# Kernel optimization log

Hardware: AMD Instinct MI355X
Metric: run time of the kernel (lower is better)

The kernel has to match this reference:

```python
import jax, jax.numpy as jnp
import numpy as np

N = 100000      # nodes
E = 800000      # edges
P = 200000      # number of subgraph permutations
L = 16          # lrp_length
D = 64          # lrp_out_dim (== lrp_in_dim)
PL = P * L
LEN_SEQ = 4     # int(sqrt(L))
NUM_BOND = 4


def setup_inputs() -> dict:
    key = jax.random.key(0)
    ks = jax.random.split(key, 16)
    inp = {}
    inp["nfeat"] = jax.random.normal(ks[0], (N, D), jnp.float32)
    inp["degs"] = jax.random.uniform(ks[1], (N,), jnp.float32) * 8.0 + 1.0
    inp["n2p_val"] = jnp.ones((PL,), jnp.float32)
    inp["e2p_val"] = jnp.ones((PL,), jnp.float32)
    inp["pool_val"] = jax.random.uniform(ks[2], (P,), jnp.float32)
    inp["weights"] = jax.random.normal(ks[3], (D, D, L), jnp.float32)
    inp["bias"] = jnp.zeros((1, D), jnp.float32)
    inp["w_deg0"] = jax.random.normal(ks[4], (2 * D, LEN_SEQ), jnp.float32) * 0.3
    inp["b_deg0"] = jnp.zeros((2 * D,), jnp.float32)
    inp["w_deg1"] = jax.random.normal(ks[5], (D, 2 * D), jnp.float32) * 0.1
    inp["b_deg1"] = jnp.zeros((D,), jnp.float32)
    inp["w_lin"] = jax.random.normal(ks[6], (D, D), jnp.float32) * 0.1
    inp["b_lin"] = jnp.zeros((D,), jnp.float32)
    inp["bond_emb"] = jax.random.normal(ks[7], (NUM_BOND, D), jnp.float32)
    inp["edge_feat_idx"] = jax.random.randint(ks[8], (E,), 0, NUM_BOND, jnp.int32)
    inp["n2p_row"] = jnp.arange(PL, dtype=jnp.int32)
    inp["n2p_col"] = jax.random.randint(ks[9], (PL,), 0, N, jnp.int32)
    inp["e2p_row"] = jnp.arange(PL, dtype=jnp.int32)
    inp["e2p_col"] = jax.random.randint(ks[10], (PL,), 0, E, jnp.int32)
    inp["pool_row"] = jax.random.randint(ks[11], (P,), 0, N, jnp.int32)
    inp["pool_col"] = jnp.arange(P, dtype=jnp.int32)
    return inp


def _spmm(row, col, val, x, m):
    # COO spmm: out[r] = sum_{nnz with row==r} val * x[col]
    return jax.ops.segment_sum(val[:, None] * x[col], row, num_segments=m)


def reference(nfeat, degs, n2p_val, e2p_val, pool_val, weights, bias,
              w_deg0, b_deg0, w_deg1, b_deg1, w_lin, b_lin, bond_emb,
              edge_feat_idx, n2p_row, n2p_col, e2p_row, e2p_col,
              pool_row, pool_col):
    n = nfeat.shape[0]
    pl = n2p_row.shape[0]
    d = weights.shape[0]
    l = weights.shape[2]
    p = pl // l
    len_seq = int(round(l ** 0.5))

    efeat = bond_emb[edge_feat_idx]                                  # [E, D]
    perm = _spmm(n2p_row, n2p_col, n2p_val, nfeat, pl) \
         + _spmm(e2p_row, e2p_col, e2p_val, efeat, pl)               # [P*L, D]
    deg_perm = _spmm(n2p_row, n2p_col, n2p_val, degs[:, None], pl)   # [P*L, 1]

    x = perm.reshape(p, l, d)                                        # [P, L, D]
    deg_sel = deg_perm.reshape(p, l)[:, ::len_seq + 1]               # [P, len_seq]

    h = jnp.einsum('pab,bca->pc', x, weights) + bias                 # [P, D]
    h = jax.nn.relu(h) @ w_lin.T + b_lin                             # linear(relu(.))

    g = jax.nn.relu(deg_sel @ w_deg0.T + b_deg0) @ w_deg1.T + b_deg1  # [P, D]
    h = h * g

    out = _spmm(pool_row, pool_col, pool_val, h, n)                  # [N, D]
    return out
```

## Files before the change

### kernel.cpp

```cpp
#include <hip/hip_runtime.h>
#include <hip/hip_bf16.h>

typedef __attribute__((ext_vector_type(8))) __bf16 bf16x8;
typedef __attribute__((ext_vector_type(4))) float floatx4;
typedef __attribute__((ext_vector_type(4))) int intx4;
typedef __attribute__((ext_vector_type(4))) unsigned uintx4;

constexpr int N_NODES = 100000;
constexpr int P_PERM  = 200000;

constexpr size_t W2F_OFF  = 0;
constexpr size_t WLF_OFF  = 131072;
constexpr size_t WD1F_OFF = 139264;
constexpr size_t BE_OFF   = 155648;
constexpr size_t NFBF_OFF = 3355648;
constexpr size_t WS_NEED_FULL = 3355648 + (size_t)N_NODES * 64 * 2;

__global__ void prep_all_kernel(float4* __restrict__ out,
                                const float* __restrict__ weights,
                                const float* __restrict__ w_lin,
                                const float* __restrict__ w_deg1,
                                const float* __restrict__ nfeat,
                                const int* __restrict__ e2p_col,
                                const int* __restrict__ edge_feat_idx,
                                __bf16* __restrict__ ws_bf) {
  int b = blockIdx.x;
  int t = threadIdx.x;
  if (b < 6250) {
    out[b * 256 + t] = make_float4(0.f, 0.f, 0.f, 0.f);
  } else if (b < 6554) {
    int i = (b - 6250) * 256 + t;
    if (i < 65536) {
      int j = i & 7, l = (i >> 3) & 63, ct = (i >> 9) & 3, ks = (i >> 11) & 1, a = i >> 12;
      int k = ks * 32 + (l >> 4) * 8 + j;
      int c = ct * 16 + (l & 15);
      ws_bf[W2F_OFF / 2 + i] = (__bf16)weights[k * 1024 + c * 16 + a];
    } else if (i < 65536 + 4096) {
      int i2 = i - 65536;
      int j = i2 & 7, l = (i2 >> 3) & 63, ct = (i2 >> 9) & 3, ks = (i2 >> 11) & 1;
      int k = ks * 32 + (l >> 4) * 8 + j;
      int c = ct * 16 + (l & 15);
      ws_bf[WLF_OFF / 2 + i2] = (__bf16)w_lin[c * 64 + k];
    } else if (i < 65536 + 4096 + 8192) {
      int i3 = i - 65536 - 4096;
      int j = i3 & 7, l = (i3 >> 3) & 63, ct = (i3 >> 9) & 3, ks = (i3 >> 11) & 3;
      int k = ks * 32 + (l >> 4) * 8 + j;
      int c = ct * 16 + (l & 15);
      ws_bf[WD1F_OFF / 2 + i3] = (__bf16)w_deg1[c * 128 + k];
    }
  } else if (b < 9679) {
    int i = (b - 6554) * 256 + t;
    if (i < N_NODES * 8) {
      float4 a = *(const float4*)(nfeat + (size_t)i * 8);
      float4 c = *(const float4*)(nfeat + (size_t)i * 8 + 4);
      bf16x8 o;
      o[0] = (__bf16)a.x; o[1] = (__bf16)a.y; o[2] = (__bf16)a.z; o[3] = (__bf16)a.w;
      o[4] = (__bf16)c.x; o[5] = (__bf16)c.y; o[6] = (__bf16)c.z; o[7] = (__bf16)c.w;
      *(bf16x8*)(ws_bf + NFBF_OFF / 2 + (size_t)i * 8) = o;
    }
  } else {
    int i = (b - 9679) * 256 + t;
    if (i < P_PERM * 4) {
      int4 ec = ((const int4*)e2p_col)[i];
      unsigned v = (unsigned)(edge_feat_idx[ec.x] & 0xff)
                 | ((unsigned)(edge_feat_idx[ec.y] & 0xff) << 8)
                 | ((unsigned)(edge_feat_idx[ec.z] & 0xff) << 16)
                 | ((unsigned)(edge_feat_idx[ec.w] & 0xff) << 24);
      ((unsigned*)((char*)ws_bf + BE_OFF))[i] = v;
    }
  }
}

template <bool BF16FEAT>
__global__ __launch_bounds__(256, 4) void lrp_mfma_kernel(
    const float* __restrict__ nfeat,
    const float* __restrict__ degs,
    const float* __restrict__ n2p_val,
    const float* __restrict__ e2p_val,
    const float* __restrict__ pool_val,
    const float* __restrict__ bias,
    const float* __restrict__ w_deg0,
    const float* __restrict__ b_deg0,
    const float* __restrict__ b_deg1,
    const float* __restrict__ b_lin,
    const float* __restrict__ bond_emb,
    const int* __restrict__ n2p_col,
    const int* __restrict__ pool_row,
    const __bf16* __restrict__ ws_bf,
    float* __restrict__ out) {
  __shared__ __align__(16) char shbig[18432];
  char (* const fraglds)[8192] = (char(*)[8192])shbig;
  __bf16 (* const hs)[2][16][72] = (__bf16(*)[2][16][72])shbig;
  __shared__ __align__(16) __bf16 sbond[4][72];
  __shared__ __align__(16) float swdeg0[128][4];
  __shared__ float sbd0[128];
  __shared__ float sbias[64];
  __shared__ float sblin[64];
  __shared__ float sbd1[64];

  const int t = threadIdx.x;
  const int w = t >> 6;
  const int l = t & 63;
  const int m = l & 15;
  const int q = l >> 4;
  const int pbase = blockIdx.x * 128 + w * 32;
  int pb[2]  = {pbase, pbase + 16};
  bool valid[2];
  int pbc[2];
  #pragma unroll
  for (int pt = 0; pt < 2; ++pt) {
    valid[pt] = pb[pt] < P_PERM;
    pbc[pt] = valid[pt] ? pb[pt] : (P_PERM - 16);
  }

  if (t < 256) sbond[t >> 6][t & 63] = (__bf16)bond_emb[t];
  if (t < 128) {
    *(float4*)&swdeg0[t][0] = *(const float4*)(w_deg0 + t * 4);
    sbd0[t] = b_deg0[t];
  } else if (t < 192) {
    int c = t - 128;
    sbias[c] = bias[c]; sblin[c] = b_lin[c]; sbd1[c] = b_deg1[c];
  }

  const __bf16* __restrict__ nfbf = ws_bf + NFBF_OFF / 2;
  const bf16x8* __restrict__ WLv  = (const bf16x8*)(ws_bf + WLF_OFF / 2);
  const bf16x8* __restrict__ WD1v = (const bf16x8*)(ws_bf + WD1F_OFF / 2);
  const unsigned* __restrict__ bep = (const unsigned*)((const char*)ws_bf + BE_OFF);
  const char* __restrict__ W2bytes = (const char*)ws_bf + W2F_OFF;

  intx4 nvx[2], evx[2], ncx[2];
  int bex[2];
  #pragma unroll
  for (int pt = 0; pt < 2; ++pt) {
    size_t rb = (size_t)pbc[pt] * 16;
    nvx[pt] = *(const intx4*)(n2p_val + rb + 4 * l);
    evx[pt] = *(const intx4*)(e2p_val + rb + 4 * l);
    ncx[pt] = *(const intx4*)(n2p_col + rb + 4 * l);
    bex[pt] = (int)bep[(size_t)pbc[pt] * 4 + l];
  }
  const int selbase = m * 16;

  auto stage = [&](int a, int buf) {
    #pragma unroll
    for (int j = 0; j < 2; ++j) {
      const char* g = W2bytes + (size_t)a * 8192 + (w * 2 + j) * 1024 + l * 16;
      char* lds = &fraglds[buf][(w * 2 + j) * 1024];
      __builtin_amdgcn_global_load_lds(
          (const __attribute__((address_space(1))) unsigned*)g,
          (__attribute__((address_space(3))) unsigned*)lds, 16, 0, 0);
    }
  };
  auto gath = [&](int nc, bf16x8* g) {
    #pragma unroll
    for (int ks = 0; ks < 2; ++ks) {
      int k0 = ks * 32 + q * 8;
      if (BF16FEAT) {
        g[ks] = *(const bf16x8*)(nfbf + (size_t)nc * 64 + k0);
      } else {
        float4 n0 = *(const float4*)(nfeat + (size_t)nc * 64 + k0);
        float4 n1 = *(const float4*)(nfeat + (size_t)nc * 64 + k0 + 4);
        bf16x8 o;
        o[0] = (__bf16)n0.x; o[1] = (__bf16)n0.y; o[2] = (__bf16)n0.z; o[3] = (__bf16)n0.w;
        o[4] = (__bf16)n1.x; o[5] = (__bf16)n1.y; o[6] = (__bf16)n1.z; o[7] = (__bf16)n1.w;
        g[ks] = o;
      }
    }
  };

  floatx4 acc[2][4] = {};
  float dsreg[2][4];
  float nv0[2], ev0[2];
  int nc0[2], be0[2];
  bf16x8 g_cur[2][2], g_nxt[2][2];

  #pragma unroll
  for (int pt = 0; pt < 2; ++pt) {
    nv0[pt] = __int_as_float(__builtin_amdgcn_ds_bpermute(selbase, nvx[pt][0]));
    ev0[pt] = __int_as_float(__builtin_amdgcn_ds_bpermute(selbase, evx[pt][0]));
    nc0[pt] = __builtin_amdgcn_ds_bpermute(selbase, ncx[pt][0]);
    be0[pt] = (__builtin_amdgcn_ds_bpermute(selbase, bex[pt])) & 0xff;
    gath(nc0[pt], g_cur[pt]);
  }
  stage(0, 0);
  __syncthreads();

  #pragma unroll
  for (int a = 0; a < 16; ++a) {
    const int buf = a & 1;
    float nv1[2], ev1[2];
    int nc1[2], be1[2];
    if (a < 15) {
      const int an = a + 1;
      const int sel1 = selbase + (an >> 2) * 4;
      const int sl = an & 3;
      #pragma unroll
      for (int pt = 0; pt < 2; ++pt) {
        nv1[pt] = __int_as_float(__builtin_amdgcn_ds_bpermute(sel1, nvx[pt][sl]));
        ev1[pt] = __int_as_float(__builtin_amdgcn_ds_bpermute(sel1, evx[pt][sl]));
        nc1[pt] = __builtin_amdgcn_ds_bpermute(sel1, ncx[pt][sl]);
        be1[pt] = (__builtin_amdgcn_ds_bpermute(sel1, bex[pt]) >> (sl * 8)) & 0xff;
      }
      stage(a + 1, buf ^ 1);
      #pragma unroll
      for (int pt = 0; pt < 2; ++pt) gath(nc1[pt], g_nxt[pt]);
    }

    bf16x8 afv[2][2];
    #pragma unroll
    for (int pt = 0; pt < 2; ++pt) {
      #pragma unroll
      for (int ks = 0; ks < 2; ++ks) {
        bf16x8 eb = *(const bf16x8*)&sbond[be0[pt]][ks * 32 + q * 8];
        bf16x8 af;
        #pragma unroll
        for (int j = 0; j < 8; ++j)
          af[j] = (__bf16)fmaf(nv0[pt], (float)g_cur[pt][ks][j],
                               ev0[pt] * (float)eb[j]);
        afv[pt][ks] = af;
      }
    }
    #pragma unroll
    for (int ks = 0; ks < 2; ++ks)
      #pragma unroll
      for (int ct = 0; ct < 4; ++ct) {
        bf16x8 frag = *(const bf16x8*)&fraglds[buf][((ks * 4 + ct) * 64 + l) * 16];
        acc[0][ct] = __builtin_amdgcn_mfma_f32_16x16x32_bf16(afv[0][ks], frag, acc[0][ct], 0, 0, 0);
        acc[1][ct] = __builtin_amdgcn_mfma_f32_16x16x32_bf16(afv[1][ks], frag, acc[1][ct], 0, 0, 0);
      }

    if (a == 0 || a == 5 || a == 10 || a == 15) {
      const int jj = a / 5;
      #pragma unroll
      for (int pt = 0; pt < 2; ++pt)
        dsreg[pt][jj] = nv0[pt] * degs[nc0[pt]];
    }

    if (a < 15) {
      __syncthreads();
      #pragma unroll
      for (int pt = 0; pt < 2; ++pt) {
        nv0[pt] = nv1[pt]; ev0[pt] = ev1[pt]; nc0[pt] = nc1[pt]; be0[pt] = be1[pt];
        g_cur[pt][0] = g_nxt[pt][0]; g_cur[pt][1] = g_nxt[pt][1];
      }
    }
  }

  __syncthreads();

  floatx4 acc2[2][4] = {};
  {
    #pragma unroll
    for (int pt = 0; pt < 2; ++pt)
      #pragma unroll
      for (int ct = 0; ct < 4; ++ct) {
        float bv = sbias[ct * 16 + m];
        #pragma unroll
        for (int rr = 0; rr < 4; ++rr)
          hs[w][pt][q * 4 + rr][ct * 16 + m] =
              (__bf16)fmaxf(acc[pt][ct][rr] + bv, 0.0f);
      }
    #pragma unroll
    for (int pt = 0; pt < 2; ++pt)
      #pragma unroll
      for (int ks = 0; ks < 2; ++ks) {
        bf16x8 af2 = *(const bf16x8*)&hs[w][pt][m][ks * 32 + q * 8];
        #pragma unroll
        for (int ct = 0; ct < 4; ++ct) {
          bf16x8 frag = WLv[(ks * 4 + ct) * 64 + l];
          acc2[pt][ct] = __builtin_amdgcn_mfma_f32_16x16x32_bf16(af2, frag, acc2[pt][ct], 0, 0, 0);
        }
      }
  }

  floatx4 gacc[2][4] = {};
  #pragma unroll
  for (int ks = 0; ks < 4; ++ks) {
    const int k0 = ks * 32 + q * 8;
    bf16x8 af[2];
    #pragma unroll
    for (int j = 0; j < 8; ++j) {
      int k = k0 + j;
      float4 wr = *(const float4*)&swdeg0[k][0];
      float bk = sbd0[k];
      #pragma unroll
      for (int pt = 0; pt < 2; ++pt) {
        float v = bk;
        v = fmaf(dsreg[pt][0], wr.x, v);
        v = fmaf(dsreg[pt][1], wr.y, v);
        v = fmaf(dsreg[pt][2], wr.z, v);
        v = fmaf(dsreg[pt][3], wr.w, v);
        af[pt][j] = (__bf16)fmaxf(v, 0.0f);
      }
    }
    #pragma unroll
    for (int ct = 0; ct < 4; ++ct) {
      bf16x8 frag = WD1v[(ks * 4 + ct) * 64 + l];
      gacc[0][ct] = __builtin_amdgcn_mfma_f32_16x16x32_bf16(af[0], frag, gacc[0][ct], 0, 0, 0);
      gacc[1][ct] = __builtin_amdgcn_mfma_f32_16x16x32_bf16(af[1], frag, gacc[1][ct], 0, 0, 0);
    }
  }

  #pragma unroll
  for (int pt = 0; pt < 2; ++pt) {
    if (!valid[pt]) continue;
    intx4   pr4 = *(const intx4*)(pool_row + pb[pt] + q * 4);
    floatx4 pv4 = *(const floatx4*)(pool_val + pb[pt] + q * 4);
    #pragma unroll
    for (int rr = 0; rr < 4; ++rr) {
      float* orow = out + (size_t)pr4[rr] * 64;
      float pv = pv4[rr];
      #pragma unroll
      for (int ct = 0; ct < 4; ++ct) {
        float h2 = (acc2[pt][ct][rr] + sblin[ct * 16 + m]) *
                   (gacc[pt][ct][rr] + sbd1[ct * 16 + m]);
        atomicAdd(orow + ct * 16 + m, pv * h2);
      }
    }
  }
}

extern "C" void kernel_launch(void* const* d_in, const int* in_sizes, int n_in,
                              void* d_out, int out_size, void* d_ws, size_t ws_size,
                              hipStream_t stream) {
  const float* nfeat    = (const float*)d_in[0];
  const float* degs     = (const float*)d_in[1];
  const float* n2p_val  = (const float*)d_in[2];
  const float* e2p_val  = (const float*)d_in[3];
  const float* pool_val = (const float*)d_in[4];
  const float* weights  = (const float*)d_in[5];
  const float* bias     = (const float*)d_in[6];
  const float* w_deg0   = (const float*)d_in[7];
  const float* b_deg0   = (const float*)d_in[8];
  const float* w_deg1   = (const float*)d_in[9];
  const float* b_deg1   = (const float*)d_in[10];
  const float* w_lin    = (const float*)d_in[11];
  const float* b_lin    = (const float*)d_in[12];
  const float* bond_emb = (const float*)d_in[13];
  const int* edge_feat_idx = (const int*)d_in[14];
  const int* n2p_col    = (const int*)d_in[16];
  const int* e2p_col    = (const int*)d_in[18];
  const int* pool_row   = (const int*)d_in[19];

  float* out = (float*)d_out;
  __bf16* ws_bf = (__bf16*)d_ws;

  prep_all_kernel<<<12804, 256, 0, stream>>>((float4*)out, weights, w_lin,
                                             w_deg1, nfeat, e2p_col,
                                             edge_feat_idx, ws_bf);

  int grid = (P_PERM + 127) / 128;
  if (ws_size >= WS_NEED_FULL) {
    lrp_mfma_kernel<true><<<grid, 256, 0, stream>>>(
        nfeat, degs, n2p_val, e2p_val, pool_val, bias, w_deg0, b_deg0,
        b_deg1, b_lin, bond_emb, n2p_col, pool_row, ws_bf, out);
  } else {
    lrp_mfma_kernel<false><<<grid, 256, 0, stream>>>(
        nfeat, degs, n2p_val, e2p_val, pool_val, bias, w_deg0, b_deg0,
        b_deg1, b_lin, bond_emb, n2p_col, pool_row, ws_bf, out);
  }
}
```

Measured before the change: 296.8 us.

## Deepen gather prefetch to two stages with explicit vmcnt barrier

Node-feature gathers are now issued two iterations ahead using a double-buffered register array, instead of one ahead. The full __syncthreads is replaced by an s_waitcnt vmcnt(4) plus s_barrier, so the most recent gathers can stay in flight across the barrier. The degree loads are deferred until after the main loop so they no longer stall it. This raises register pressure and depends on the hand-written vmcnt count matching the number of outstanding loads, which is fragile if the compiler reorders memory operations.

```diff
diff --git a/kernel.cpp b/kernel.cpp
--- a/kernel.cpp
+++ b/kernel.cpp
@@ -168,18 +168,21 @@
   };
 
   floatx4 acc[2][4] = {};
-  float dsreg[2][4];
+  float dsnv[2][4];
+  int dsnc[2][4];
   float nv0[2], ev0[2];
-  int nc0[2], be0[2];
-  bf16x8 g_cur[2][2], g_nxt[2][2];
+  int be0[2];
+  bf16x8 g[2][2][2];
 
   #pragma unroll
   for (int pt = 0; pt < 2; ++pt) {
     nv0[pt] = __int_as_float(__builtin_amdgcn_ds_bpermute(selbase, nvx[pt][0]));
     ev0[pt] = __int_as_float(__builtin_amdgcn_ds_bpermute(selbase, evx[pt][0]));
-    nc0[pt] = __builtin_amdgcn_ds_bpermute(selbase, ncx[pt][0]);
     be0[pt] = (__builtin_amdgcn_ds_bpermute(selbase, bex[pt])) & 0xff;
-    gath(nc0[pt], g_cur[pt]);
+    int nc0p = __builtin_amdgcn_ds_bpermute(selbase, ncx[pt][0]);
+    gath(nc0p, g[0][pt]);
+    int nc1p = __builtin_amdgcn_ds_bpermute(selbase, ncx[pt][1]);
+    gath(nc1p, g[1][pt]);
   }
   stage(0, 0);
   __syncthreads();
@@ -188,7 +191,7 @@
   for (int a = 0; a < 16; ++a) {
     const int buf = a & 1;
     float nv1[2], ev1[2];
-    int nc1[2], be1[2];
+    int be1[2];
     if (a < 15) {
       const int an = a + 1;
       const int sel1 = selbase + (an >> 2) * 4;
@@ -197,12 +200,9 @@
       for (int pt = 0; pt < 2; ++pt) {
         nv1[pt] = __int_as_float(__builtin_amdgcn_ds_bpermute(sel1, nvx[pt][sl]));
         ev1[pt] = __int_as_float(__builtin_amdgcn_ds_bpermute(sel1, evx[pt][sl]));
-        nc1[pt] = __builtin_amdgcn_ds_bpermute(sel1, ncx[pt][sl]);
         be1[pt] = (__builtin_amdgcn_ds_bpermute(sel1, bex[pt]) >> (sl * 8)) & 0xff;
       }
       stage(a + 1, buf ^ 1);
-      #pragma unroll
-      for (int pt = 0; pt < 2; ++pt) gath(nc1[pt], g_nxt[pt]);
     }
 
     bf16x8 afv[2][2];
@@ -214,7 +214,7 @@
         bf16x8 af;
         #pragma unroll
         for (int j = 0; j < 8; ++j)
-          af[j] = (__bf16)fmaf(nv0[pt], (float)g_cur[pt][ks][j],
+          af[j] = (__bf16)fmaf(nv0[pt], (float)g[buf][pt][ks][j],
                                ev0[pt] * (float)eb[j]);
         afv[pt][ks] = af;
       }
@@ -230,20 +230,49 @@
 
     if (a == 0 || a == 5 || a == 10 || a == 15) {
       const int jj = a / 5;
+      const int seld = selbase + (a >> 2) * 4;
+      const int sd = a & 3;
+      #pragma unroll
+      for (int pt = 0; pt < 2; ++pt) {
+        dsnv[pt][jj] = nv0[pt];
+        dsnc[pt][jj] = __builtin_amdgcn_ds_bpermute(seld, ncx[pt][sd]);
+      }
+    }
+
+    if (a < 14) {
+      const int a2 = a + 2;
+      const int sel2 = selbase + (a2 >> 2) * 4;
+      const int s2 = a2 & 3;
+      int nc2[2];
       #pragma unroll
       for (int pt = 0; pt < 2; ++pt)
-        dsreg[pt][jj] = nv0[pt] * degs[nc0[pt]];
+        nc2[pt] = __builtin_amdgcn_ds_bpermute(sel2, ncx[pt][s2]);
+      __builtin_amdgcn_sched_barrier(0);
+      #pragma unroll
+      for (int pt = 0; pt < 2; ++pt) gath(nc2[pt], g[buf][pt]);
+    } else {
+      __builtin_amdgcn_sched_barrier(0);
     }
 
     if (a < 15) {
-      __syncthreads();
+      if (a == 14) {
+        asm volatile("s_waitcnt vmcnt(0)\n\ts_barrier" ::: "memory");
+      } else {
+        asm volatile("s_waitcnt vmcnt(4)\n\ts_barrier" ::: "memory");
+      }
       #pragma unroll
       for (int pt = 0; pt < 2; ++pt) {
-        nv0[pt] = nv1[pt]; ev0[pt] = ev1[pt]; nc0[pt] = nc1[pt]; be0[pt] = be1[pt];
-        g_cur[pt][0] = g_nxt[pt][0]; g_cur[pt][1] = g_nxt[pt][1];
-      }
-    }
-  }
+        nv0[pt] = nv1[pt]; ev0[pt] = ev1[pt]; be0[pt] = be1[pt];
+      }
+    }
+  }
+
+  float dsreg[2][4];
+  #pragma unroll
+  for (int pt = 0; pt < 2; ++pt)
+    #pragma unroll
+    for (int jj = 0; jj < 4; ++jj)
+      dsreg[pt][jj] = dsnv[pt][jj] * degs[dsnc[pt][jj]];
 
   __syncthreads();
 
```

Result: no change. 299.0 us (+0.7%).
